# Performance work log

Measured on AMD Instinct MI355X. Metric: run time of the kernel, lower is better.

## Reference

```python
import jax, jax.numpy as jnp
import numpy as np

C_M = 256
C = 32
C_Z = 128
EPS = 1e-5


def setup_inputs() -> dict:
    key = jax.random.key(0)
    ks = jax.random.split(key, 8)
    b, s, i = 1, 128, 256
    msa = jax.random.normal(ks[0], (b, s, i, C_M), dtype=jnp.float32)
    scale_in = 1.0 / np.sqrt(C_M)
    scale_out = 1.0 / np.sqrt(C * C)
    return {
        "msa_representation": msa,
        "ln_w": jnp.ones((C_M,), jnp.float32),
        "ln_b": jnp.zeros((C_M,), jnp.float32),
        "w_left": jax.random.normal(ks[1], (C_M, C), jnp.float32) * scale_in,
        "b_left": jax.random.normal(ks[2], (C,), jnp.float32) * scale_in,
        "w_right": jax.random.normal(ks[3], (C_M, C), jnp.float32) * scale_in,
        "b_right": jax.random.normal(ks[4], (C,), jnp.float32) * scale_in,
        "w_out": jax.random.normal(ks[5], (C * C, C_Z), jnp.float32) * scale_out,
        "b_out": jax.random.normal(ks[6], (C_Z,), jnp.float32) * scale_out,
    }


def reference(msa_representation, ln_w, ln_b, w_left, b_left, w_right, b_right, w_out, b_out):
    x = msa_representation
    # LayerNorm over c_m
    mu = jnp.mean(x, axis=-1, keepdims=True)
    var = jnp.mean(jnp.square(x - mu), axis=-1, keepdims=True)
    x = (x - mu) * jax.lax.rsqrt(var + EPS) * ln_w + ln_b
    # dual projections: [b, s, i, c]
    A = x @ w_left + b_left
    B = x @ w_right + b_right
    s_dim = x.shape[1]
    # outer product mean over MSA depth s: [b, i, j, c, c]
    outer = jnp.einsum('bsic,bsjd->bijcd', A, B) / s_dim
    b_, i_, j_ = outer.shape[0], outer.shape[1], outer.shape[2]
    flat = outer.reshape(b_, i_, j_, C * C)
    return flat @ w_out + b_out
```

## Files before the change

### kernel.cpp

```cpp
#include <hip/hip_runtime.h>

typedef __attribute__((ext_vector_type(8))) short short8;
typedef __attribute__((ext_vector_type(4))) float f32x4;

#define CM 256
#define CC 32
#define CZ 128
#define SDIM 128
#define IDIM 256

__device__ __forceinline__ unsigned short f2bf(float f) {
  union { float f; unsigned u; } v; v.f = f;
  unsigned r = v.u + 0x7fffu + ((v.u >> 16) & 1u);
  return (unsigned short)(r >> 16);
}
__device__ __forceinline__ unsigned pack_bf2(float a, float b) {
  union { float f; unsigned u; } x, y; x.f = a; y.f = b;
  return ((x.u + 0x8000u) >> 16) | ((y.u + 0x8000u) & 0xffff0000u);
}

__global__ void k_prep(const float* __restrict__ wl, const float* __restrict__ wr,
                       const float* __restrict__ wo,
                       unsigned short* __restrict__ wlrT2, unsigned short* __restrict__ WF) {
  int t = blockIdx.x * 256 + threadIdx.x;
  if (t < 2048) {
    int frag = t >> 6, lane = t & 63;
    int nt = frag >> 3, ks = frag & 7;
    int ln = lane & 15, qd = lane >> 4;
    int c64 = nt * 16 + ln;
#pragma unroll
    for (int e = 0; e < 8; ++e) {
      int cm = ks * 32 + qd * 8 + e;
      float v = (c64 < CC) ? wl[cm * CC + c64] : wr[cm * CC + (c64 - CC)];
      wlrT2[(size_t)t * 8 + e] = f2bf(v);
    }
  } else {
    int t2 = t - 2048;
    if (t2 < 8 * 32 * 64) {
      int zt = t2 >> 11, ks = (t2 >> 6) & 31, lane = t2 & 63;
      int ln = lane & 15, qd = lane >> 4;
      int z = zt * 16 + ln;
#pragma unroll
      for (int e = 0; e < 8; ++e) {
        int c = qd * 8 + e, d = ks;
        WF[(size_t)t2 * 8 + e] = f2bf(wo[(c * 32 + d) * CZ + z] * (1.0f / 128.0f));
      }
    }
  }
}

__global__ __launch_bounds__(256) void k_lnproj(
    const float* __restrict__ x, const float* __restrict__ lnw, const float* __restrict__ lnb,
    const float* __restrict__ bl, const float* __restrict__ br,
    const unsigned short* __restrict__ wlrT2,
    unsigned short* __restrict__ A2, unsigned short* __restrict__ Bbuf) {
  __shared__ __align__(16) unsigned short xn[64][264];
  __shared__ __align__(16) unsigned short sT[64][72];
  int tid = threadIdx.x;
  int lane = tid & 63, ww = tid >> 6;
  int qd = lane >> 4, ln = lane & 15;
  int i = blockIdx.x, sh = blockIdx.y;

  for (int rr = 0; rr < 16; ++rr) {
    int sl = ww * 16 + rr;
    int s = sh * 64 + sl;
    float4 v = ((const float4*)(x + ((size_t)s * IDIM + i) * CM))[lane];
    float s1 = v.x + v.y + v.z + v.w;
    float s2 = v.x * v.x + v.y * v.y + v.z * v.z + v.w * v.w;
#pragma unroll
    for (int off = 32; off; off >>= 1) {
      s1 += __shfl_xor(s1, off);
      s2 += __shfl_xor(s2, off);
    }
    float mu = s1 * (1.0f / 256.0f);
    float var = s2 * (1.0f / 256.0f) - mu * mu;
    float rs = rsqrtf(var + 1e-5f);
    float4 w4 = ((const float4*)lnw)[lane];
    float4 b4 = ((const float4*)lnb)[lane];
    ushort4 h;
    h.x = f2bf((v.x - mu) * rs * w4.x + b4.x);
    h.y = f2bf((v.y - mu) * rs * w4.y + b4.y);
    h.z = f2bf((v.z - mu) * rs * w4.z + b4.z);
    h.w = f2bf((v.w - mu) * rs * w4.w + b4.w);
    *(ushort4*)&xn[sl][lane * 4] = h;
  }
  __syncthreads();

  f32x4 acc[4];
#pragma unroll
  for (int nt = 0; nt < 4; ++nt) acc[nt] = (f32x4){0.f, 0.f, 0.f, 0.f};
#pragma unroll
  for (int ks = 0; ks < 8; ++ks) {
    short8 af = *(const short8*)&xn[ww * 16 + ln][ks * 32 + qd * 8];
#pragma unroll
    for (int nt = 0; nt < 4; ++nt) {
      short8 bf = *(const short8*)(wlrT2 + ((size_t)((nt * 8 + ks) * 64 + lane)) * 8);
      acc[nt] = __builtin_amdgcn_mfma_f32_16x16x32_bf16(af, bf, acc[nt], 0, 0, 0);
    }
  }
#pragma unroll
  for (int nt = 0; nt < 4; ++nt) {
    int c64 = nt * 16 + ln;
    float bias = (c64 < CC) ? bl[c64] : br[c64 - CC];
    ushort4 h;
    h.x = f2bf(acc[nt][0] + bias);
    h.y = f2bf(acc[nt][1] + bias);
    h.z = f2bf(acc[nt][2] + bias);
    h.w = f2bf(acc[nt][3] + bias);
    *(ushort4*)&sT[c64][ww * 16 + qd * 4] = h;
  }
  __syncthreads();

  {
    int rtloc = ww >> 1, ksl = ww & 1;
    short8 v = *(const short8*)&sT[rtloc * 16 + ln][ksl * 32 + qd * 8];
    *(short8*)(A2 + ((size_t)(((2 * i + rtloc) * 4 + (sh * 2 + ksl)) * 64 + lane)) * 8) = v;
  }
  {
    int row = tid >> 3, ch = tid & 7;
    short8 v = *(const short8*)&sT[CC + row][ch * 8];
    *(short8*)(Bbuf + ((size_t)(i * CC + row)) * SDIM + sh * 64 + ch * 8) = v;
  }
}

__global__ __launch_bounds__(1024) void k_main(
    const unsigned short* __restrict__ A2, const unsigned short* __restrict__ Bbuf,
    const unsigned short* __restrict__ WF, const float* __restrict__ bout,
    float* __restrict__ out) {
  extern __shared__ __align__(16) char lds[];
  unsigned short* sB = (unsigned short*)lds;
  unsigned short* sP = (unsigned short*)lds;
  float* redR = (float*)lds;
  int tid = threadIdx.x;
  int lane = tid & 63, ww = tid >> 6;
  int qd = lane >> 4, ln = lane & 15;
  int i0 = blockIdx.x * 8, j0 = blockIdx.y * 8;

#pragma unroll
  for (int t = 0; t < 4; ++t) {
    int idx = tid + t * 1024;
    int r = idx >> 4, ch = idx & 15;
    short8 v = *(const short8*)(Bbuf + (size_t)(j0 * CC + r) * SDIM + ch * 8);
    *(short8*)&sB[r * 136 + ch * 8] = v;
  }
  __syncthreads();

  int wy = ww >> 2, wx = ww & 3;
  f32x4 acc1[4][4];
#pragma unroll
  for (int a = 0; a < 4; ++a)
#pragma unroll
    for (int b = 0; b < 4; ++b) acc1[a][b] = (f32x4){0.f, 0.f, 0.f, 0.f};
#pragma unroll
  for (int ks = 0; ks < 4; ++ks) {
    short8 af[4];
#pragma unroll
    for (int ti = 0; ti < 4; ++ti)
      af[ti] = *(const short8*)(A2 + ((size_t)((i0 * 2 + wy * 4 + ti) * 4 + ks) * 64 + lane) * 8);
#pragma unroll
    for (int tj = 0; tj < 4; ++tj) {
      short8 bf = *(const short8*)&sB[(wx * 64 + tj * 16 + ln) * 136 + ks * 32 + qd * 8];
#pragma unroll
      for (int ti = 0; ti < 4; ++ti)
        acc1[ti][tj] = __builtin_amdgcn_mfma_f32_16x16x32_bf16(af[ti], bf, acc1[ti][tj], 0, 0, 0);
    }
  }
  __syncthreads();

#pragma unroll
  for (int ti = 0; ti < 4; ++ti) {
    int iloc = wy * 2 + (ti >> 1);
    int cbase = 16 * (ti & 1) + qd * 4;
    int cb = cbase >> 3;
#pragma unroll
    for (int tj = 0; tj < 4; ++tj) {
      int jloc = wx * 2 + (tj >> 1);
      int d = 16 * (tj & 1) + ln;
      int p = iloc * 8 + jloc;
      uint2 u;
      u.x = pack_bf2(acc1[ti][tj][0], acc1[ti][tj][1]);
      u.y = pack_bf2(acc1[ti][tj][2], acc1[ti][tj][3]);
      *(uint2*)&sP[p * 1032 + d * 32 + ((((d >> 1) & 3) ^ cb) * 8) + (cbase & 7)] = u;
    }
  }
  __syncthreads();

  int ztp = ww & 3, kq = ww >> 2;
  f32x4 acc2[2][4];
#pragma unroll
  for (int a = 0; a < 2; ++a)
#pragma unroll
    for (int b = 0; b < 4; ++b) acc2[a][b] = (f32x4){0.f, 0.f, 0.f, 0.f};
#pragma unroll
  for (int cc = 0; cc < 8; ++cc) {
    int ks = kq * 8 + cc;
    short8 afr[4];
#pragma unroll
    for (int mt = 0; mt < 4; ++mt)
      afr[mt] = *(const short8*)&sP[(mt * 16 + ln) * 1032 + ks * 32 + ((((ks >> 1) & 3) ^ qd) * 8)];
#pragma unroll
    for (int h2 = 0; h2 < 2; ++h2) {
      int zt = ztp * 2 + h2;
      short8 bfr = *(const short8*)(WF + ((size_t)(zt * 32 + ks) * 64 + lane) * 8);
#pragma unroll
      for (int mt = 0; mt < 4; ++mt)
        acc2[h2][mt] = __builtin_amdgcn_mfma_f32_16x16x32_bf16(bfr, afr[mt], acc2[h2][mt], 0, 0, 0);
    }
  }

  __syncthreads();
  if (kq >= 2) {
    int s = (kq - 2) * 4 + ztp;
#pragma unroll
    for (int h2 = 0; h2 < 2; ++h2)
#pragma unroll
      for (int mt = 0; mt < 4; ++mt)
        *(f32x4*)&redR[(((s * 2 + h2) * 4 + mt) << 8) + lane * 4] = acc2[h2][mt];
  }
  __syncthreads();
  if (kq < 2) {
    int s = kq * 4 + ztp;
#pragma unroll
    for (int h2 = 0; h2 < 2; ++h2)
#pragma unroll
      for (int mt = 0; mt < 4; ++mt)
        acc2[h2][mt] += *(const f32x4*)&redR[(((s * 2 + h2) * 4 + mt) << 8) + lane * 4];
  }
  __syncthreads();
  if (kq == 1) {
    int s = ztp;
#pragma unroll
    for (int h2 = 0; h2 < 2; ++h2)
#pragma unroll
      for (int mt = 0; mt < 4; ++mt)
        *(f32x4*)&redR[(((s * 2 + h2) * 4 + mt) << 8) + lane * 4] = acc2[h2][mt];
  }
  __syncthreads();
  if (kq == 0) {
    int s = ztp;
#pragma unroll
    for (int h2 = 0; h2 < 2; ++h2) {
      int z = (ztp * 2 + h2) * 16 + qd * 4;
      f32x4 bz = *(const f32x4*)(bout + z);
#pragma unroll
      for (int mt = 0; mt < 4; ++mt) {
        int p = mt * 16 + ln;
        f32x4 v = acc2[h2][mt] +
                  *(const f32x4*)&redR[(((s * 2 + h2) * 4 + mt) << 8) + lane * 4] + bz;
        int i = i0 + (p >> 3), j = j0 + (p & 7);
        *(f32x4*)&out[((size_t)i * IDIM + j) * CZ + z] = v;
      }
    }
  }
}

extern "C" void kernel_launch(void* const* d_in, const int* in_sizes, int n_in,
                              void* d_out, int out_size, void* d_ws, size_t ws_size,
                              hipStream_t stream) {
  const float* msa = (const float*)d_in[0];
  const float* lnw = (const float*)d_in[1];
  const float* lnb = (const float*)d_in[2];
  const float* wl  = (const float*)d_in[3];
  const float* bl  = (const float*)d_in[4];
  const float* wr  = (const float*)d_in[5];
  const float* br  = (const float*)d_in[6];
  const float* wo  = (const float*)d_in[7];
  const float* bo  = (const float*)d_in[8];
  float* out = (float*)d_out;

  char* ws = (char*)d_ws;
  unsigned short* A2    = (unsigned short*)ws;
  unsigned short* Bbuf  = (unsigned short*)(ws + (2u << 20));
  unsigned short* wlrT2 = (unsigned short*)(ws + (4u << 20));
  unsigned short* WF    = (unsigned short*)(ws + (4u << 20) + 32768);

  (void)hipFuncSetAttribute((const void*)k_main,
                            hipFuncAttributeMaxDynamicSharedMemorySize, 132096);

  k_prep<<<72, 256, 0, stream>>>(wl, wr, wo, wlrT2, WF);
  k_lnproj<<<dim3(256, 2), 256, 0, stream>>>(msa, lnw, lnb, bl, br, wlrT2, A2, Bbuf);
  k_main<<<dim3(32, 32), 1024, 132096, stream>>>(A2, Bbuf, WF, bo, out);
}
```

Baseline: 143.3 us.

## Loop each block over four j-tiles, keeping A and W fragments in registers

The main kernel now launches 256 blocks, each handling four consecutive 8-wide j tiles, instead of one block per (i,j) tile. The A fragments and the W_out fragments are loaded into registers once and reused across the four tiles. The next tile's B slice is prefetched from global memory while the current tile computes. The reduction buffer moves to a separate LDS region so the barriers around it can be reduced. The cost is much higher register pressure (32 extra short8 per thread at 1024 threads) and fewer blocks to spread across CUs, which risks spills or lower occupancy.

```diff
diff --git a/kernel.cpp b/kernel.cpp
--- a/kernel.cpp
+++ b/kernel.cpp
@@ -130,125 +130,165 @@
   extern __shared__ __align__(16) char lds[];
   unsigned short* sB = (unsigned short*)lds;
   unsigned short* sP = (unsigned short*)lds;
-  float* redR = (float*)lds;
+  float* redR = (float*)(lds + 69632);
   int tid = threadIdx.x;
   int lane = tid & 63, ww = tid >> 6;
   int qd = lane >> 4, ln = lane & 15;
-  int i0 = blockIdx.x * 8, j0 = blockIdx.y * 8;
-
-#pragma unroll
+  int bx = blockIdx.x;
+  int bi = (bx & 7) * 4 + ((bx >> 3) & 3);
+  int bjg = bx >> 5;
+  int i0 = bi * 8;
+  int wy = ww >> 2, wx = ww & 3;
+  int ztp = ww & 3, kq = ww >> 2;
+
+  short8 afA[16];
+  short8 wreg[16];
+  short8 bpre[4];
+
+#pragma unroll
+  for (int tt = 0; tt < 4; ++tt) {
+    int idx = tid + tt * 1024;
+    int r = idx >> 4, ch = idx & 15;
+    bpre[tt] = *(const short8*)(Bbuf + ((size_t)(bjg * 4) * 256 + r) * SDIM + ch * 8);
+  }
+#pragma unroll
+  for (int ti = 0; ti < 4; ++ti)
+#pragma unroll
+    for (int ks = 0; ks < 4; ++ks)
+      afA[ti * 4 + ks] =
+          *(const short8*)(A2 + ((size_t)((i0 * 2 + wy * 4 + ti) * 4 + ks) * 64 + lane) * 8);
+#pragma unroll
+  for (int h2 = 0; h2 < 2; ++h2)
+#pragma unroll
+    for (int cc = 0; cc < 8; ++cc)
+      wreg[h2 * 8 + cc] = *(const short8*)(
+          WF + ((size_t)((ztp * 2 + h2) * 32 + kq * 8 + cc) * 64 + lane) * 8);
+#pragma unroll
+  for (int tt = 0; tt < 4; ++tt) {
+    int idx = tid + tt * 1024;
+    int r = idx >> 4, ch = idx & 15;
+    *(short8*)&sB[r * 136 + ch * 8] = bpre[tt];
+  }
+  __syncthreads();
+
   for (int t = 0; t < 4; ++t) {
-    int idx = tid + t * 1024;
-    int r = idx >> 4, ch = idx & 15;
-    short8 v = *(const short8*)(Bbuf + (size_t)(j0 * CC + r) * SDIM + ch * 8);
-    *(short8*)&sB[r * 136 + ch * 8] = v;
-  }
-  __syncthreads();
-
-  int wy = ww >> 2, wx = ww & 3;
-  f32x4 acc1[4][4];
-#pragma unroll
-  for (int a = 0; a < 4; ++a)
-#pragma unroll
-    for (int b = 0; b < 4; ++b) acc1[a][b] = (f32x4){0.f, 0.f, 0.f, 0.f};
-#pragma unroll
-  for (int ks = 0; ks < 4; ++ks) {
-    short8 af[4];
-#pragma unroll
-    for (int ti = 0; ti < 4; ++ti)
-      af[ti] = *(const short8*)(A2 + ((size_t)((i0 * 2 + wy * 4 + ti) * 4 + ks) * 64 + lane) * 8);
-#pragma unroll
-    for (int tj = 0; tj < 4; ++tj) {
-      short8 bf = *(const short8*)&sB[(wx * 64 + tj * 16 + ln) * 136 + ks * 32 + qd * 8];
-#pragma unroll
-      for (int ti = 0; ti < 4; ++ti)
-        acc1[ti][tj] = __builtin_amdgcn_mfma_f32_16x16x32_bf16(af[ti], bf, acc1[ti][tj], 0, 0, 0);
-    }
-  }
-  __syncthreads();
-
-#pragma unroll
-  for (int ti = 0; ti < 4; ++ti) {
-    int iloc = wy * 2 + (ti >> 1);
-    int cbase = 16 * (ti & 1) + qd * 4;
-    int cb = cbase >> 3;
-#pragma unroll
-    for (int tj = 0; tj < 4; ++tj) {
-      int jloc = wx * 2 + (tj >> 1);
-      int d = 16 * (tj & 1) + ln;
-      int p = iloc * 8 + jloc;
-      uint2 u;
-      u.x = pack_bf2(acc1[ti][tj][0], acc1[ti][tj][1]);
-      u.y = pack_bf2(acc1[ti][tj][2], acc1[ti][tj][3]);
-      *(uint2*)&sP[p * 1032 + d * 32 + ((((d >> 1) & 3) ^ cb) * 8) + (cbase & 7)] = u;
-    }
-  }
-  __syncthreads();
-
-  int ztp = ww & 3, kq = ww >> 2;
-  f32x4 acc2[2][4];
-#pragma unroll
-  for (int a = 0; a < 2; ++a)
-#pragma unroll
-    for (int b = 0; b < 4; ++b) acc2[a][b] = (f32x4){0.f, 0.f, 0.f, 0.f};
-#pragma unroll
-  for (int cc = 0; cc < 8; ++cc) {
-    int ks = kq * 8 + cc;
-    short8 afr[4];
-#pragma unroll
-    for (int mt = 0; mt < 4; ++mt)
-      afr[mt] = *(const short8*)&sP[(mt * 16 + ln) * 1032 + ks * 32 + ((((ks >> 1) & 3) ^ qd) * 8)];
-#pragma unroll
-    for (int h2 = 0; h2 < 2; ++h2) {
-      int zt = ztp * 2 + h2;
-      short8 bfr = *(const short8*)(WF + ((size_t)(zt * 32 + ks) * 64 + lane) * 8);
+    int jt = bjg * 4 + t;
+    int j0 = jt * 8;
+
+    if (t < 3) {
+#pragma unroll
+      for (int tt = 0; tt < 4; ++tt) {
+        int idx = tid + tt * 1024;
+        int r = idx >> 4, ch = idx & 15;
+        bpre[tt] = *(const short8*)(Bbuf + ((size_t)(jt + 1) * 256 + r) * SDIM + ch * 8);
+      }
+    }
+
+    f32x4 acc1[4][4];
+#pragma unroll
+    for (int a = 0; a < 4; ++a)
+#pragma unroll
+      for (int b = 0; b < 4; ++b) acc1[a][b] = (f32x4){0.f, 0.f, 0.f, 0.f};
+#pragma unroll
+    for (int ks = 0; ks < 4; ++ks)
+#pragma unroll
+      for (int tj = 0; tj < 4; ++tj) {
+        short8 bf = *(const short8*)&sB[(wx * 64 + tj * 16 + ln) * 136 + ks * 32 + qd * 8];
+#pragma unroll
+        for (int ti = 0; ti < 4; ++ti)
+          acc1[ti][tj] =
+              __builtin_amdgcn_mfma_f32_16x16x32_bf16(afA[ti * 4 + ks], bf, acc1[ti][tj], 0, 0, 0);
+      }
+    __syncthreads();
+
+#pragma unroll
+    for (int ti = 0; ti < 4; ++ti) {
+      int iloc = wy * 2 + (ti >> 1);
+      int cbase = 16 * (ti & 1) + qd * 4;
+      int cb = cbase >> 3;
+#pragma unroll
+      for (int tj = 0; tj < 4; ++tj) {
+        int jloc = wx * 2 + (tj >> 1);
+        int d = 16 * (tj & 1) + ln;
+        int p = iloc * 8 + jloc;
+        uint2 u;
+        u.x = pack_bf2(acc1[ti][tj][0], acc1[ti][tj][1]);
+        u.y = pack_bf2(acc1[ti][tj][2], acc1[ti][tj][3]);
+        *(uint2*)&sP[p * 1032 + d * 32 + ((((d >> 1) & 3) ^ cb) * 8) + (cbase & 7)] = u;
+      }
+    }
+    __syncthreads();
+
+    f32x4 acc2[2][4];
+#pragma unroll
+    for (int a = 0; a < 2; ++a)
+#pragma unroll
+      for (int b = 0; b < 4; ++b) acc2[a][b] = (f32x4){0.f, 0.f, 0.f, 0.f};
+#pragma unroll
+    for (int cc = 0; cc < 8; ++cc) {
+      int ks = kq * 8 + cc;
+      short8 afr[4];
 #pragma unroll
       for (int mt = 0; mt < 4; ++mt)
-        acc2[h2][mt] = __builtin_amdgcn_mfma_f32_16x16x32_bf16(bfr, afr[mt], acc2[h2][mt], 0, 0, 0);
-    }
-  }
-
-  __syncthreads();
-  if (kq >= 2) {
-    int s = (kq - 2) * 4 + ztp;
-#pragma unroll
-    for (int h2 = 0; h2 < 2; ++h2)
-#pragma unroll
-      for (int mt = 0; mt < 4; ++mt)
-        *(f32x4*)&redR[(((s * 2 + h2) * 4 + mt) << 8) + lane * 4] = acc2[h2][mt];
-  }
-  __syncthreads();
-  if (kq < 2) {
-    int s = kq * 4 + ztp;
-#pragma unroll
-    for (int h2 = 0; h2 < 2; ++h2)
-#pragma unroll
-      for (int mt = 0; mt < 4; ++mt)
-        acc2[h2][mt] += *(const f32x4*)&redR[(((s * 2 + h2) * 4 + mt) << 8) + lane * 4];
-  }
-  __syncthreads();
-  if (kq == 1) {
-    int s = ztp;
-#pragma unroll
-    for (int h2 = 0; h2 < 2; ++h2)
-#pragma unroll
-      for (int mt = 0; mt < 4; ++mt)
-        *(f32x4*)&redR[(((s * 2 + h2) * 4 + mt) << 8) + lane * 4] = acc2[h2][mt];
-  }
-  __syncthreads();
-  if (kq == 0) {
-    int s = ztp;
-#pragma unroll
-    for (int h2 = 0; h2 < 2; ++h2) {
-      int z = (ztp * 2 + h2) * 16 + qd * 4;
-      f32x4 bz = *(const f32x4*)(bout + z);
-#pragma unroll
-      for (int mt = 0; mt < 4; ++mt) {
-        int p = mt * 16 + ln;
-        f32x4 v = acc2[h2][mt] +
-                  *(const f32x4*)&redR[(((s * 2 + h2) * 4 + mt) << 8) + lane * 4] + bz;
-        int i = i0 + (p >> 3), j = j0 + (p & 7);
-        *(f32x4*)&out[((size_t)i * IDIM + j) * CZ + z] = v;
+        afr[mt] =
+            *(const short8*)&sP[(mt * 16 + ln) * 1032 + ks * 32 + ((((ks >> 1) & 3) ^ qd) * 8)];
+#pragma unroll
+      for (int h2 = 0; h2 < 2; ++h2)
+#pragma unroll
+        for (int mt = 0; mt < 4; ++mt)
+          acc2[h2][mt] = __builtin_amdgcn_mfma_f32_16x16x32_bf16(wreg[h2 * 8 + cc], afr[mt],
+                                                                acc2[h2][mt], 0, 0, 0);
+    }
+    __syncthreads();
+
+    if (t < 3) {
+#pragma unroll
+      for (int tt = 0; tt < 4; ++tt) {
+        int idx = tid + tt * 1024;
+        int r = idx >> 4, ch = idx & 15;
+        *(short8*)&sB[r * 136 + ch * 8] = bpre[tt];
+      }
+    }
+    if (kq >= 2) {
+      int s = (kq - 2) * 4 + ztp;
+#pragma unroll
+      for (int h2 = 0; h2 < 2; ++h2)
+#pragma unroll
+        for (int mt = 0; mt < 4; ++mt)
+          *(f32x4*)&redR[(((s * 2 + h2) * 4 + mt) << 8) + lane * 4] = acc2[h2][mt];
+    }
+    __syncthreads();
+    if (kq < 2) {
+      int s = kq * 4 + ztp;
+#pragma unroll
+      for (int h2 = 0; h2 < 2; ++h2)
+#pragma unroll
+        for (int mt = 0; mt < 4; ++mt)
+          acc2[h2][mt] += *(const f32x4*)&redR[(((s * 2 + h2) * 4 + mt) << 8) + lane * 4];
+    }
+    if (kq == 1) {
+      int s = 4 + ztp;
+#pragma unroll
+      for (int h2 = 0; h2 < 2; ++h2)
+#pragma unroll
+        for (int mt = 0; mt < 4; ++mt)
+          *(f32x4*)&redR[(((s * 2 + h2) * 4 + mt) << 8) + lane * 4] = acc2[h2][mt];
+    }
+    __syncthreads();
+    if (kq == 0) {
+      int s = 4 + ztp;
+#pragma unroll
+      for (int h2 = 0; h2 < 2; ++h2) {
+        int z = (ztp * 2 + h2) * 16 + qd * 4;
+        f32x4 bz = *(const f32x4*)(bout + z);
+#pragma unroll
+        for (int mt = 0; mt < 4; ++mt) {
+          int p = mt * 16 + ln;
+          f32x4 v = acc2[h2][mt] +
+                    *(const f32x4*)&redR[(((s * 2 + h2) * 4 + mt) << 8) + lane * 4] + bz;
+          int i = i0 + (p >> 3), j = j0 + (p & 7);
+          *(f32x4*)&out[((size_t)i * IDIM + j) * CZ + z] = v;
+        }
       }
     }
   }
@@ -275,9 +315,9 @@
   unsigned short* WF    = (unsigned short*)(ws + (4u << 20) + 32768);
 
   (void)hipFuncSetAttribute((const void*)k_main,
-                            hipFuncAttributeMaxDynamicSharedMemorySize, 132096);
+                            hipFuncAttributeMaxDynamicSharedMemorySize, 135168);
 
   k_prep<<<72, 256, 0, stream>>>(wl, wr, wo, wlrT2, WF);
   k_lnproj<<<dim3(256, 2), 256, 0, stream>>>(msa, lnw, lnb, bl, br, wlrT2, A2, Bbuf);
-  k_main<<<dim3(32, 32), 1024, 132096, stream>>>(A2, Bbuf, WF, bo, out);
-}
+  k_main<<<256, 1024, 135168, stream>>>(A2, Bbuf, WF, bo, out);
+}
```

After: 246.2 us. 71.9% more time.
